# Kernel tuning notes

Measured on AMD Instinct MI355X. Metric: run time of the kernel, lower is better.

Reference implementation:

```python
import jax, jax.numpy as jnp
import numpy as np

N_ATOMS = 64
N_FEA = 64
N_RBF = 64
RBF_GAP = 0.1
N_INT = 3
BATCH = 512
P = N_ATOMS * (N_ATOMS - 1)  # 4032 ordered pairs (fully connected graph)

# pair index lists exactly as in the torch module
IDX_I = np.hstack([[k] * (N_ATOMS - 1) for k in range(N_ATOMS)])
IDX_J = np.hstack([list(range(0, k)) + list(range(k + 1, N_ATOMS)) for k in range(N_ATOMS)])


def setup_inputs() -> dict:
    key = jax.random.key(0)
    ks = jax.random.split(key, 20)
    sc_v = np.sqrt(1.0 / np.sqrt(N_FEA)).astype(np.float32)  # init scale from the module

    def lin(k, fan_in, shape):
        return jax.random.normal(k, shape, dtype=jnp.float32) / np.sqrt(fan_in)

    return {
        "r": jax.random.normal(ks[0], (BATCH, N_ATOMS * 3), dtype=jnp.float32),
        "v1": sc_v * jax.random.normal(ks[1], (N_FEA,), dtype=jnp.float32),
        "v2": sc_v * jax.random.normal(ks[2], (N_FEA,), dtype=jnp.float32),
        "rbf_centers": jnp.arange(N_RBF, dtype=jnp.float32) * 0.15625,
        # interaction-block linears, stacked over the 3 interactions; stored (in, out)
        "Wx": lin(ks[3], N_FEA, (N_INT, N_FEA, N_FEA)),
        "bx": jnp.zeros((N_INT, N_FEA), jnp.float32),
        "Wf1": lin(ks[4], N_RBF, (N_INT, N_RBF, N_FEA)),
        "bf1": jnp.zeros((N_INT, N_FEA), jnp.float32),
        "Wf2": lin(ks[5], N_FEA, (N_INT, N_FEA, N_FEA)),
        "bf2": jnp.zeros((N_INT, N_FEA), jnp.float32),
        "Wv1": lin(ks[6], N_FEA, (N_INT, N_FEA, N_FEA)),
        "bv1": jnp.zeros((N_INT, N_FEA), jnp.float32),
        "Wv2": lin(ks[7], N_FEA, (N_INT, N_FEA, N_FEA)),
        "bv2": jnp.zeros((N_INT, N_FEA), jnp.float32),
        "W1": lin(ks[8], N_FEA, (N_FEA, N_FEA // 2)),
        "b1": jnp.zeros((N_FEA // 2,), jnp.float32),
        "W2": lin(ks[9], N_FEA // 2, (N_FEA // 2, 1)),
        "b2": jnp.zeros((1,), jnp.float32),
    }


def reference(r, v1, v2, rbf_centers, Wx, bx, Wf1, bf1, Wf2, bf2,
              Wv1, bv1, Wv2, bv2, W1, b1, W2, b2):
    act = jnp.tanh
    b = r.shape[0]
    pos = r.reshape(b, N_ATOMS, 3)

    # pairwise distances (get_wrapvec = identity, no PBC)
    diff = pos[:, IDX_I] - pos[:, IDX_J]                      # (b, P, 3)
    dij = jnp.linalg.norm(diff, axis=-1, keepdims=True)       # (b, P, 1)
    rbf = jnp.exp(-(dij - rbf_centers) ** 2 / RBF_GAP)        # (b, P, R)

    # initial atom embeddings: atoms 0,1 -> v1; atoms 2.. -> v2
    x0 = jnp.concatenate([jnp.broadcast_to(v1, (2, N_FEA)),
                          jnp.broadcast_to(v2, (N_ATOMS - 2, N_FEA))], axis=0)
    X = jnp.broadcast_to(x0, (b, N_ATOMS, N_FEA))

    for t in range(N_INT):
        Xl = X @ Wx[t] + bx[t]                                # atom-wise linear
        h = act(rbf @ Wf1[t] + bf1[t])                        # filter network on RBF
        h = act(h @ Wf2[t] + bf2[t])                          # (b, P, F)
        v = h * Xl[:, IDX_J]                                  # gather neighbor feats, cfconv
        v = v.reshape(b, N_ATOMS, N_ATOMS - 1, N_FEA).sum(axis=2)  # scatter-sum over j
        v = act(v @ Wv1[t] + bv1[t])
        v = v @ Wv2[t] + bv2[t]
        X = X + v

    X = act(X @ W1 + b1)
    X = X @ W2 + b2                                           # (b, n_atoms, 1)
    return jnp.sum(X[..., 0], axis=-1, keepdims=True)         # (b, 1)
```

## Files before the change

kernel.cpp:

```cpp
#include <hip/hip_runtime.h>


typedef __attribute__((ext_vector_type(8))) __bf16 bf16x8;
typedef __attribute__((ext_vector_type(4))) __bf16 bf16x4;
typedef __attribute__((ext_vector_type(4))) float  f32x4;

#define WS_X  262144
#define WS_V  8650752
#define WS_XL 12845056

__device__ __forceinline__ int swz(int row, int byteoff) {
    return row * 128 + (byteoff ^ ((row & 7) << 4));
}

__device__ __forceinline__ float fexp2(float x) { return __builtin_amdgcn_exp2f(x); }

__device__ __forceinline__ float tanh_fast(float x) {
    float t = fexp2(2.88539008f * x);
    return fmaf(-2.0f, __builtin_amdgcn_rcpf(t + 1.0f), 1.0f);
}

struct AFrag { bf16x8 a0h, a1h, a0l, a1l; };

__device__ __forceinline__ AFrag load_afrag(const char* wsW, int mat, int wv, int lane) {
    const char* p = wsW + mat * 16384 + wv * 2048 + lane * 32;
    AFrag f;
    f.a0h = *(const bf16x8*)(p);
    f.a1h = *(const bf16x8*)(p + 16);
    f.a0l = *(const bf16x8*)(p + 8192);
    f.a1l = *(const bf16x8*)(p + 8192 + 16);
    return f;
}

template <int EPI, bool BSPLIT>
__device__ __forceinline__ void gemm64(const AFrag& A, const char* Bhi, const char* Blo,
                                       const f32x4 bv, char* Out,
                                       int lane, int wv, f32x4* ret) {
    const int l15 = lane & 15, q = lane >> 4;
    f32x4 acc[4];
#pragma unroll
    for (int nt = 0; nt < 4; ++nt) {
        const int n = 16 * nt + l15;
        const bf16x8 b0h = *(const bf16x8*)(Bhi + swz(n, 16 * q));
        const bf16x8 b1h = *(const bf16x8*)(Bhi + swz(n, 64 + 16 * q));
        f32x4 c = {0.f, 0.f, 0.f, 0.f};
        c = __builtin_amdgcn_mfma_f32_16x16x32_bf16(A.a0h, b0h, c, 0, 0, 0);
        c = __builtin_amdgcn_mfma_f32_16x16x32_bf16(A.a1h, b1h, c, 0, 0, 0);
        c = __builtin_amdgcn_mfma_f32_16x16x32_bf16(A.a0l, b0h, c, 0, 0, 0);
        c = __builtin_amdgcn_mfma_f32_16x16x32_bf16(A.a1l, b1h, c, 0, 0, 0);
        if (BSPLIT) {
            const bf16x8 b0l = *(const bf16x8*)(Blo + swz(n, 16 * q));
            const bf16x8 b1l = *(const bf16x8*)(Blo + swz(n, 64 + 16 * q));
            c = __builtin_amdgcn_mfma_f32_16x16x32_bf16(A.a0h, b0l, c, 0, 0, 0);
            c = __builtin_amdgcn_mfma_f32_16x16x32_bf16(A.a1h, b1l, c, 0, 0, 0);
        }
        acc[nt] = c;
    }
    if (EPI == 2) {
#pragma unroll
        for (int nt = 0; nt < 4; ++nt) ret[nt] = acc[nt];
        return;
    }
#pragma unroll
    for (int nt = 0; nt < 4; ++nt) {
        const int n = 16 * nt + l15;
        bf16x4 oh;
#pragma unroll
        for (int r = 0; r < 4; ++r) {
            float v = acc[nt][r] + bv[r];
            if (EPI == 1) v = tanh_fast(v);
            oh[r] = (__bf16)v;
        }
        *(bf16x4*)(Out + swz(n, 32 * wv + 8 * q)) = oh;
    }
}

__global__ void prep_weights(const float* __restrict__ Wx, const float* __restrict__ Wf1,
                             const float* __restrict__ Wf2, const float* __restrict__ Wv1,
                             const float* __restrict__ Wv2, const float* __restrict__ W1,
                             char* __restrict__ ws) {
    const int m = blockIdx.x;
    const int tid = threadIdx.x;
    const int wv = tid >> 6, lane = tid & 63;
    const int l15 = lane & 15, q = lane >> 4;
    const int m_row = 16 * wv + l15;
    const float* src;
    int wcols;
    if (m < 15) {
        const int t = m / 5, s = m % 5;
        src = (s == 0 ? Wx : s == 1 ? Wf1 : s == 2 ? Wf2 : s == 3 ? Wv1 : Wv2) + t * 4096;
        wcols = 64;
    } else {
        src = W1;
        wcols = 32;
    }
    char* base = ws + m * 16384 + wv * 2048 + lane * 32;
#pragma unroll
    for (int kc = 0; kc < 2; ++kc) {
        bf16x8 hi, lo;
#pragma unroll
        for (int e = 0; e < 8; ++e) {
            const int k = 32 * kc + 8 * q + e;
            float val = (m_row < wcols) ? src[k * wcols + m_row] : 0.0f;
            __bf16 h = (__bf16)val;
            hi[e] = h;
            lo[e] = (__bf16)(val - (float)h);
        }
        *(bf16x8*)(base + kc * 16) = hi;
        *(bf16x8*)(base + 8192 + kc * 16) = lo;
    }
}

__global__ __launch_bounds__(256, 2) void schnet_init(
    const float* __restrict__ v1g, const float* __restrict__ v2g,
    const float* __restrict__ bx,  const char* __restrict__ wsW,
    float* __restrict__ gX, __bf16* __restrict__ gXl) {
    extern __shared__ char smem[];
    char* bX   = smem;
    char* bXlo = smem + 8192;

    const int tid = threadIdx.x;
    const int lane = tid & 63, wv = tid >> 6;
    const int l15 = lane & 15, q = lane >> 4;
    const int b = blockIdx.x;

    {
        const f32x4 a1v = *(const f32x4*)(v1g + 16 * wv + 4 * q);
        const f32x4 a2v = *(const f32x4*)(v2g + 16 * wv + 4 * q);
#pragma unroll
        for (int nt = 0; nt < 4; ++nt) {
            const bool isv1 = (nt == 0) && (l15 < 2);
            bf16x4 oh, ol;
            f32x4 m;
#pragma unroll
            for (int rr = 0; rr < 4; ++rr) {
                m[rr] = isv1 ? a1v[rr] : a2v[rr];
                __bf16 h = (__bf16)m[rr];
                oh[rr] = h;
                ol[rr] = (__bf16)(m[rr] - (float)h);
            }
            const int off = swz(16 * nt + l15, 32 * wv + 8 * q);
            *(bf16x4*)(bX + off) = oh;
            *(bf16x4*)(bXlo + off) = ol;
            *(f32x4*)(gX + b * 4096 + (16 * nt + l15) * 64 + 16 * wv + 4 * q) = m;
        }
    }
    __syncthreads();
    {
        const AFrag fWx = load_afrag(wsW, 0, wv, lane);
        const f32x4 bxv = *(const f32x4*)(bx + 16 * wv + 4 * q);
        f32x4 acc[4];
        gemm64<2, true>(fWx, bX, bXlo, bxv, nullptr, lane, wv, acc);
#pragma unroll
        for (int nt = 0; nt < 4; ++nt) {
            bf16x4 oh;
#pragma unroll
            for (int rr = 0; rr < 4; ++rr) oh[rr] = (__bf16)(acc[nt][rr] + bxv[rr]);
            *(bf16x4*)(gXl + (b * 64 + 16 * nt + l15) * 64 + 16 * wv + 4 * q) = oh;
        }
    }
}

__global__ __launch_bounds__(256, 4) void schnet_a(
    const float* __restrict__ r,   const float* __restrict__ cent,
    const float* __restrict__ bf1, const float* __restrict__ bf2,
    const char* __restrict__ wsW,  const __bf16* __restrict__ gXl,
    __bf16* __restrict__ gV, int t) {
    extern __shared__ char smem[];
    char* bA  = smem;
    char* bB  = smem + 8192;
    float* sPos  = (float*)(smem + 16384);
    float* sCent = (float*)(smem + 17152);

    const int tid = threadIdx.x;
    const int lane = tid & 63, wv = tid >> 6;
    const int l15 = lane & 15, q = lane >> 4;
    const int b = blockIdx.x >> 2, qh = blockIdx.x & 3;

    if (tid < 192) sPos[(tid % 3) * 64 + tid / 3] = r[b * 192 + tid];
    if (tid < 64) sCent[tid] = cent[tid];

    const AFrag fWf1 = load_afrag(wsW, t * 5 + 1, wv, lane);
    const AFrag fWf2 = load_afrag(wsW, t * 5 + 2, wv, lane);
    const f32x4 bf1v = *(const f32x4*)(bf1 + t * 64 + 16 * wv + 4 * q);
    const f32x4 bf2v = *(const f32x4*)(bf2 + t * 64 + 16 * wv + 4 * q);

    float xlf[4][4];
#pragma unroll
    for (int nt = 0; nt < 4; ++nt) {
        const bf16x4 xl = *(const bf16x4*)(gXl + (b * 64 + 16 * nt + l15) * 64 +
                                           16 * wv + 4 * q);
#pragma unroll
        for (int r2 = 0; r2 < 4; ++r2) xlf[nt][r2] = (float)xl[r2];
    }
    __syncthreads();

    const float pjx = sPos[lane], pjy = sPos[64 + lane], pjz = sPos[128 + lane];
    const float* ccp = sCent + wv * 16;

    const int i0 = qh * 16;
    {
        const float dx = pjx - sPos[i0];
        const float dy = pjy - sPos[64 + i0];
        const float dz = pjz - sPos[128 + i0];
        const float d = __builtin_amdgcn_sqrtf(dx * dx + dy * dy + dz * dz);
        bf16x8 h0, h1v;
#pragma unroll
        for (int e = 0; e < 8; ++e) {
            float x0 = d - ccp[e];
            float x1 = d - ccp[8 + e];
            h0[e]  = (__bf16)fexp2(-14.4269504f * x0 * x0);
            h1v[e] = (__bf16)fexp2(-14.4269504f * x1 * x1);
        }
        *(bf16x8*)(bA + swz(lane, 32 * wv)) = h0;
        *(bf16x8*)(bA + swz(lane, 32 * wv + 16)) = h1v;
    }
    __syncthreads();

    for (int ii = 0; ii < 16; ++ii) {
        const int i = i0 + ii;
        gemm64<1, false>(fWf1, bA, nullptr, bf1v, bB, lane, wv, nullptr);
        __syncthreads();
        {
            f32x4 ret[4];
            gemm64<2, false>(fWf2, bB, nullptr, bf2v, nullptr, lane, wv, ret);
            float ts0 = 0.f, ts1 = 0.f, ts2 = 0.f, ts3 = 0.f;
#pragma unroll
            for (int nt = 0; nt < 4; ++nt) {
                const int j = 16 * nt + l15;
                const bool valid = (j != i);
                ts0 = fmaf(tanh_fast(ret[nt][0] + bf2v[0]), valid ? xlf[nt][0] : 0.f, ts0);
                ts1 = fmaf(tanh_fast(ret[nt][1] + bf2v[1]), valid ? xlf[nt][1] : 0.f, ts1);
                ts2 = fmaf(tanh_fast(ret[nt][2] + bf2v[2]), valid ? xlf[nt][2] : 0.f, ts2);
                ts3 = fmaf(tanh_fast(ret[nt][3] + bf2v[3]), valid ? xlf[nt][3] : 0.f, ts3);
            }
#pragma unroll
            for (int m = 1; m < 16; m <<= 1) {
                ts0 += __shfl_xor(ts0, m);
                ts1 += __shfl_xor(ts1, m);
                ts2 += __shfl_xor(ts2, m);
                ts3 += __shfl_xor(ts3, m);
            }
            if (l15 == 0) {
                bf16x4 o;
                o[0] = (__bf16)ts0; o[1] = (__bf16)ts1;
                o[2] = (__bf16)ts2; o[3] = (__bf16)ts3;
                *(bf16x4*)(gV + (b * 64 + i) * 64 + 16 * wv + 4 * q) = o;
            }
        }
        if (ii < 15) {
            const int inext = i + 1;
            const float dx = pjx - sPos[inext];
            const float dy = pjy - sPos[64 + inext];
            const float dz = pjz - sPos[128 + inext];
            const float d = __builtin_amdgcn_sqrtf(dx * dx + dy * dy + dz * dz);
            bf16x8 h0, h1v;
#pragma unroll
            for (int e = 0; e < 8; ++e) {
                float x0 = d - ccp[e];
                float x1 = d - ccp[8 + e];
                h0[e]  = (__bf16)fexp2(-14.4269504f * x0 * x0);
                h1v[e] = (__bf16)fexp2(-14.4269504f * x1 * x1);
            }
            *(bf16x8*)(bA + swz(lane, 32 * wv)) = h0;
            *(bf16x8*)(bA + swz(lane, 32 * wv + 16)) = h1v;
        }
        __syncthreads();
    }
}

__global__ __launch_bounds__(256, 2) void schnet_b(
    const float* __restrict__ bv1, const float* __restrict__ bv2,
    const float* __restrict__ bx,  const float* __restrict__ b1,
    const float* __restrict__ W2,  const float* __restrict__ b2,
    const char* __restrict__ wsW,  float* __restrict__ gX,
    const __bf16* __restrict__ gV, __bf16* __restrict__ gXl,
    float* __restrict__ out, int t) {
    extern __shared__ char smem[];
    char* bV   = smem;
    char* bB   = smem + 8192;
    char* bX   = smem + 16384;
    char* bXlo = smem + 24576;
    float* sRed = (float*)(smem + 32768);
    float* sW2v = (float*)(smem + 33280);

    const int tid = threadIdx.x;
    const int lane = tid & 63, wv = tid >> 6;
    const int l15 = lane & 15, q = lane >> 4;
    const int b = blockIdx.x;

    if (tid < 32) sW2v[tid] = W2[tid];

    {
        const int a = tid >> 2, f0 = (tid & 3) << 4;
        const __bf16* src = gV + (b * 64 + a) * 64 + f0;
        const bf16x8 v0 = *(const bf16x8*)(src);
        const bf16x8 v1 = *(const bf16x8*)(src + 8);
        *(bf16x8*)(bV + swz(a, 2 * f0)) = v0;
        *(bf16x8*)(bV + swz(a, 2 * f0 + 16)) = v1;
    }
    __syncthreads();
    {
        const AFrag fWv1 = load_afrag(wsW, t * 5 + 3, wv, lane);
        const f32x4 bv1v = *(const f32x4*)(bv1 + t * 64 + 16 * wv + 4 * q);
        gemm64<1, false>(fWv1, bV, nullptr, bv1v, bB, lane, wv, nullptr);
    }
    __syncthreads();
    f32x4 master[4];
    {
        const AFrag fWv2 = load_afrag(wsW, t * 5 + 4, wv, lane);
        f32x4 ret[4];
        gemm64<2, false>(fWv2, bB, nullptr, f32x4{0.f, 0.f, 0.f, 0.f}, nullptr,
                         lane, wv, ret);
        const f32x4 bvec = *(const f32x4*)(bv2 + t * 64 + 16 * wv + 4 * q);
#pragma unroll
        for (int nt = 0; nt < 4; ++nt) {
            float* px = gX + b * 4096 + (16 * nt + l15) * 64 + 16 * wv + 4 * q;
            f32x4 m = *(const f32x4*)px;
#pragma unroll
            for (int rr = 0; rr < 4; ++rr) m[rr] += ret[nt][rr] + bvec[rr];
            *(f32x4*)px = m;
            master[nt] = m;
            bf16x4 oh, ol;
#pragma unroll
            for (int rr = 0; rr < 4; ++rr) {
                __bf16 h = (__bf16)m[rr];
                oh[rr] = h;
                ol[rr] = (__bf16)(m[rr] - (float)h);
            }
            const int off = swz(16 * nt + l15, 32 * wv + 8 * q);
            *(bf16x4*)(bX + off) = oh;
            *(bf16x4*)(bXlo + off) = ol;
        }
    }
    __syncthreads();

    if (t < 2) {
        const AFrag fWxn = load_afrag(wsW, (t + 1) * 5 + 0, wv, lane);
        const f32x4 bxv = *(const f32x4*)(bx + (t + 1) * 64 + 16 * wv + 4 * q);
        f32x4 acc[4];
        gemm64<2, true>(fWxn, bX, bXlo, bxv, nullptr, lane, wv, acc);
#pragma unroll
        for (int nt = 0; nt < 4; ++nt) {
            bf16x4 oh;
#pragma unroll
            for (int rr = 0; rr < 4; ++rr) oh[rr] = (__bf16)(acc[nt][rr] + bxv[rr]);
            *(bf16x4*)(gXl + (b * 64 + 16 * nt + l15) * 64 + 16 * wv + 4 * q) = oh;
        }
    } else {
        if (wv < 2) {
            const AFrag fW1 = load_afrag(wsW, 15, wv, lane);
            const f32x4 b1v = *(const f32x4*)(b1 + 16 * wv + 4 * q);
            const f32x4 w2v = *(const f32x4*)(sW2v + 16 * wv + 4 * q);
#pragma unroll
            for (int nt = 0; nt < 4; ++nt) {
                const int n = 16 * nt + l15;
                const bf16x8 b0h = *(const bf16x8*)(bX + swz(n, 16 * q));
                const bf16x8 b1h = *(const bf16x8*)(bX + swz(n, 64 + 16 * q));
                const bf16x8 b0l = *(const bf16x8*)(bXlo + swz(n, 16 * q));
                const bf16x8 b1l = *(const bf16x8*)(bXlo + swz(n, 64 + 16 * q));
                f32x4 c = {0.f, 0.f, 0.f, 0.f};
                c = __builtin_amdgcn_mfma_f32_16x16x32_bf16(fW1.a0h, b0h, c, 0, 0, 0);
                c = __builtin_amdgcn_mfma_f32_16x16x32_bf16(fW1.a1h, b1h, c, 0, 0, 0);
                c = __builtin_amdgcn_mfma_f32_16x16x32_bf16(fW1.a0h, b0l, c, 0, 0, 0);
                c = __builtin_amdgcn_mfma_f32_16x16x32_bf16(fW1.a1h, b1l, c, 0, 0, 0);
                c = __builtin_amdgcn_mfma_f32_16x16x32_bf16(fW1.a0l, b0h, c, 0, 0, 0);
                c = __builtin_amdgcn_mfma_f32_16x16x32_bf16(fW1.a1l, b1h, c, 0, 0, 0);
                float p = 0.f;
#pragma unroll
                for (int rr = 0; rr < 4; ++rr)
                    p = fmaf(tanh_fast(c[rr] + b1v[rr]), w2v[rr], p);
                p += __shfl_xor(p, 16);
                p += __shfl_xor(p, 32);
                if (q == 0) sRed[wv * 64 + nt * 16 + l15] = p;
            }
        }
        __syncthreads();
        if (tid < 64) {
            float s = sRed[tid] + sRed[64 + tid];
#pragma unroll
            for (int off = 1; off < 64; off <<= 1) s += __shfl_xor(s, off);
            if (tid == 0) out[b] = s + 64.0f * b2[0];
        }
    }
}

extern "C" void kernel_launch(void* const* d_in, const int* in_sizes, int n_in,
                              void* d_out, int out_size, void* d_ws, size_t ws_size,
                              hipStream_t stream) {
    const float* r    = (const float*)d_in[0];
    const float* v1   = (const float*)d_in[1];
    const float* v2   = (const float*)d_in[2];
    const float* cent = (const float*)d_in[3];
    const float* Wx   = (const float*)d_in[4];
    const float* bx   = (const float*)d_in[5];
    const float* Wf1  = (const float*)d_in[6];
    const float* bf1  = (const float*)d_in[7];
    const float* Wf2  = (const float*)d_in[8];
    const float* bf2  = (const float*)d_in[9];
    const float* Wv1  = (const float*)d_in[10];
    const float* bv1  = (const float*)d_in[11];
    const float* Wv2  = (const float*)d_in[12];
    const float* bv2  = (const float*)d_in[13];
    const float* W1   = (const float*)d_in[14];
    const float* b1   = (const float*)d_in[15];
    const float* W2   = (const float*)d_in[16];
    const float* b2   = (const float*)d_in[17];
    char* ws = (char*)d_ws;
    float*  gX  = (float*)(ws + WS_X);
    __bf16* gV  = (__bf16*)(ws + WS_V);
    __bf16* gXl = (__bf16*)(ws + WS_XL);

    prep_weights<<<16, 256, 0, stream>>>(Wx, Wf1, Wf2, Wv1, Wv2, W1, ws);
    schnet_init<<<512, 256, 16384, stream>>>(v1, v2, bx, ws, gX, gXl);

    (void)hipFuncSetAttribute((const void*)schnet_a,
                              hipFuncAttributeMaxDynamicSharedMemorySize, 17408);
    (void)hipFuncSetAttribute((const void*)schnet_b,
                              hipFuncAttributeMaxDynamicSharedMemorySize, 33408);
    for (int t = 0; t < 3; ++t) {
        schnet_a<<<2048, 256, 17408, stream>>>(r, cent, bf1, bf2, ws, gXl, gV, t);
        schnet_b<<<512, 256, 33408, stream>>>(bv1, bv2, bx, b1, W2, b2, ws, gX,
                                              gV, gXl, (float*)d_out, t);
    }
}
```

Before: 485.3 us.

## Exploit pair symmetry to halve filter network evaluations via cyclic offsets

Reorganizes the cfconv kernel to iterate over cyclic pair offsets instead of center atoms, so each filter evaluation h_ij (symmetric in i,j) contributes to both atom i and atom j via a lane shuffle. The grid is halved and each block accumulates per-atom partial sums in registers, written as fp32 halves that the second kernel sums. This removes half of the RBF/filter GEMM and tanh work at the cost of extra gathers, cross-lane shuffles, and doubled fp32 partial-sum traffic.

After: 856.0 us. 76.4% more time.

```diff
diff --git a/kernel.cpp b/kernel.cpp
--- a/kernel.cpp
+++ b/kernel.cpp
@@ -6,8 +6,8 @@
 typedef __attribute__((ext_vector_type(4))) float  f32x4;
 
 #define WS_X  262144
-#define WS_V  8650752
-#define WS_XL 12845056
+#define WS_XL 8650752
+#define WS_VP 12845056
 
 __device__ __forceinline__ int swz(int row, int byteoff) {
     return row * 128 + (byteoff ^ ((row & 7) << 4));
@@ -165,7 +165,7 @@
     const float* __restrict__ r,   const float* __restrict__ cent,
     const float* __restrict__ bf1, const float* __restrict__ bf2,
     const char* __restrict__ wsW,  const __bf16* __restrict__ gXl,
-    __bf16* __restrict__ gV, int t) {
+    float* __restrict__ gVp, int t) {
     extern __shared__ char smem[];
     char* bA  = smem;
     char* bB  = smem + 8192;
@@ -175,7 +175,7 @@
     const int tid = threadIdx.x;
     const int lane = tid & 63, wv = tid >> 6;
     const int l15 = lane & 15, q = lane >> 4;
-    const int b = blockIdx.x >> 2, qh = blockIdx.x & 3;
+    const int b = blockIdx.x >> 1, half = blockIdx.x & 1;
 
     if (tid < 192) sPos[(tid % 3) * 64 + tid / 3] = r[b * 192 + tid];
     if (tid < 64) sCent[tid] = cent[tid];
@@ -193,80 +193,105 @@
 #pragma unroll
         for (int r2 = 0; r2 < 4; ++r2) xlf[nt][r2] = (float)xl[r2];
     }
+    f32x4 vacc[4];
+#pragma unroll
+    for (int nt = 0; nt < 4; ++nt) vacc[nt] = f32x4{0.f, 0.f, 0.f, 0.f};
     __syncthreads();
 
     const float pjx = sPos[lane], pjy = sPos[64 + lane], pjz = sPos[128 + lane];
     const float* ccp = sCent + wv * 16;
-
-    const int i0 = qh * 16;
-    {
-        const float dx = pjx - sPos[i0];
-        const float dy = pjy - sPos[64 + i0];
-        const float dz = pjz - sPos[128 + i0];
-        const float d = __builtin_amdgcn_sqrtf(dx * dx + dy * dy + dz * dz);
-        bf16x8 h0, h1v;
-#pragma unroll
-        for (int e = 0; e < 8; ++e) {
-            float x0 = d - ccp[e];
-            float x1 = d - ccp[8 + e];
-            h0[e]  = (__bf16)fexp2(-14.4269504f * x0 * x0);
-            h1v[e] = (__bf16)fexp2(-14.4269504f * x1 * x1);
-        }
-        *(bf16x8*)(bA + swz(lane, 32 * wv)) = h0;
-        *(bf16x8*)(bA + swz(lane, 32 * wv + 16)) = h1v;
-    }
-    __syncthreads();
-
-    for (int ii = 0; ii < 16; ++ii) {
-        const int i = i0 + ii;
+    const int o0 = 1 + half * 16;
+
+#define RBF_COL(O)                                                        \
+    {                                                                     \
+        const int jj = (lane + (O)) & 63;                                 \
+        const float dx = pjx - sPos[jj];                                  \
+        const float dy = pjy - sPos[64 + jj];                             \
+        const float dz = pjz - sPos[128 + jj];                            \
+        const float d = __builtin_amdgcn_sqrtf(dx * dx + dy * dy + dz * dz); \
+        bf16x8 h0, h1v;                                                   \
+        _Pragma("unroll")                                                 \
+        for (int e = 0; e < 8; ++e) {                                     \
+            float x0 = d - ccp[e];                                        \
+            float x1 = d - ccp[8 + e];                                    \
+            h0[e]  = (__bf16)fexp2(-14.4269504f * x0 * x0);               \
+            h1v[e] = (__bf16)fexp2(-14.4269504f * x1 * x1);               \
+        }                                                                 \
+        *(bf16x8*)(bA + swz(lane, 32 * wv)) = h0;                         \
+        *(bf16x8*)(bA + swz(lane, 32 * wv + 16)) = h1v;                   \
+    }
+
+    RBF_COL(o0);
+    __syncthreads();
+
+    for (int oc = 0; oc < 16; ++oc) {
+        const int o = o0 + oc;
         gemm64<1, false>(fWf1, bA, nullptr, bf1v, bB, lane, wv, nullptr);
         __syncthreads();
         {
+            bf16x4 xjl[4];
+            if (o != 32) {
+#pragma unroll
+                for (int nt = 0; nt < 4; ++nt) {
+                    const int j = (16 * nt + l15 + o) & 63;
+                    xjl[nt] = *(const bf16x4*)(gXl + (b * 64 + j) * 64 +
+                                               16 * wv + 4 * q);
+                }
+            }
             f32x4 ret[4];
             gemm64<2, false>(fWf2, bB, nullptr, bf2v, nullptr, lane, wv, ret);
-            float ts0 = 0.f, ts1 = 0.f, ts2 = 0.f, ts3 = 0.f;
-#pragma unroll
-            for (int nt = 0; nt < 4; ++nt) {
-                const int j = 16 * nt + l15;
-                const bool valid = (j != i);
-                ts0 = fmaf(tanh_fast(ret[nt][0] + bf2v[0]), valid ? xlf[nt][0] : 0.f, ts0);
-                ts1 = fmaf(tanh_fast(ret[nt][1] + bf2v[1]), valid ? xlf[nt][1] : 0.f, ts1);
-                ts2 = fmaf(tanh_fast(ret[nt][2] + bf2v[2]), valid ? xlf[nt][2] : 0.f, ts2);
-                ts3 = fmaf(tanh_fast(ret[nt][3] + bf2v[3]), valid ? xlf[nt][3] : 0.f, ts3);
+            if (o != 32) {
+                f32x4 prod[4];
+#pragma unroll
+                for (int nt = 0; nt < 4; ++nt) {
+#pragma unroll
+                    for (int r2 = 0; r2 < 4; ++r2) {
+                        const float hv = tanh_fast(ret[nt][r2] + bf2v[r2]);
+                        vacc[nt][r2] = fmaf(hv, (float)xjl[nt][r2], vacc[nt][r2]);
+                        prod[nt][r2] = hv * xlf[nt][r2];
+                    }
+                }
+                const int srcLane = (lane & 48) | ((l15 - o) & 15);
+                f32x4 rx[4];
+#pragma unroll
+                for (int nt = 0; nt < 4; ++nt)
+#pragma unroll
+                    for (int r2 = 0; r2 < 4; ++r2)
+                        rx[nt][r2] = __shfl(prod[nt][r2], srcLane, 64);
+                const int carry = (((l15 - o) & 15) + o) >> 4;
+                if (carry == 0) {
+                    vacc[0] += rx[0]; vacc[1] += rx[1];
+                    vacc[2] += rx[2]; vacc[3] += rx[3];
+                } else if (carry == 1) {
+                    vacc[1] += rx[0]; vacc[2] += rx[1];
+                    vacc[3] += rx[2]; vacc[0] += rx[3];
+                } else {
+                    vacc[2] += rx[0]; vacc[3] += rx[1];
+                    vacc[0] += rx[2]; vacc[1] += rx[3];
+                }
+            } else {
+#pragma unroll
+                for (int nt = 0; nt < 2; ++nt) {
+#pragma unroll
+                    for (int r2 = 0; r2 < 4; ++r2) {
+                        const float hv = tanh_fast(ret[nt][r2] + bf2v[r2]);
+                        vacc[nt][r2]     = fmaf(hv, xlf[nt + 2][r2], vacc[nt][r2]);
+                        vacc[nt + 2][r2] = fmaf(hv, xlf[nt][r2], vacc[nt + 2][r2]);
+                    }
+                }
             }
-#pragma unroll
-            for (int m = 1; m < 16; m <<= 1) {
-                ts0 += __shfl_xor(ts0, m);
-                ts1 += __shfl_xor(ts1, m);
-                ts2 += __shfl_xor(ts2, m);
-                ts3 += __shfl_xor(ts3, m);
-            }
-            if (l15 == 0) {
-                bf16x4 o;
-                o[0] = (__bf16)ts0; o[1] = (__bf16)ts1;
-                o[2] = (__bf16)ts2; o[3] = (__bf16)ts3;
-                *(bf16x4*)(gV + (b * 64 + i) * 64 + 16 * wv + 4 * q) = o;
-            }
-        }
-        if (ii < 15) {
-            const int inext = i + 1;
-            const float dx = pjx - sPos[inext];
-            const float dy = pjy - sPos[64 + inext];
-            const float dz = pjz - sPos[128 + inext];
-            const float d = __builtin_amdgcn_sqrtf(dx * dx + dy * dy + dz * dz);
-            bf16x8 h0, h1v;
-#pragma unroll
-            for (int e = 0; e < 8; ++e) {
-                float x0 = d - ccp[e];
-                float x1 = d - ccp[8 + e];
-                h0[e]  = (__bf16)fexp2(-14.4269504f * x0 * x0);
-                h1v[e] = (__bf16)fexp2(-14.4269504f * x1 * x1);
-            }
-            *(bf16x8*)(bA + swz(lane, 32 * wv)) = h0;
-            *(bf16x8*)(bA + swz(lane, 32 * wv + 16)) = h1v;
-        }
+        }
+        if (oc < 15) RBF_COL(o + 1);
         __syncthreads();
     }
+
+    {
+        float* dst = gVp + (half * 512 + b) * 4096;
+#pragma unroll
+        for (int nt = 0; nt < 4; ++nt)
+            *(f32x4*)(dst + (16 * nt + l15) * 64 + 16 * wv + 4 * q) = vacc[nt];
+    }
+#undef RBF_COL
 }
 
 __global__ __launch_bounds__(256, 2) void schnet_b(
@@ -274,7 +299,7 @@
     const float* __restrict__ bx,  const float* __restrict__ b1,
     const float* __restrict__ W2,  const float* __restrict__ b2,
     const char* __restrict__ wsW,  float* __restrict__ gX,
-    const __bf16* __restrict__ gV, __bf16* __restrict__ gXl,
+    const float* __restrict__ gVp, __bf16* __restrict__ gXl,
     float* __restrict__ out, int t) {
     extern __shared__ char smem[];
     char* bV   = smem;
@@ -292,12 +317,18 @@
     if (tid < 32) sW2v[tid] = W2[tid];
 
     {
-        const int a = tid >> 2, f0 = (tid & 3) << 4;
-        const __bf16* src = gV + (b * 64 + a) * 64 + f0;
-        const bf16x8 v0 = *(const bf16x8*)(src);
-        const bf16x8 v1 = *(const bf16x8*)(src + 8);
-        *(bf16x8*)(bV + swz(a, 2 * f0)) = v0;
-        *(bf16x8*)(bV + swz(a, 2 * f0 + 16)) = v1;
+        const int a2 = tid >> 2, f0 = (tid & 3) << 4;
+        const float* s0 = gVp + b * 4096 + a2 * 64 + f0;
+        const float* s1 = gVp + (512 + b) * 4096 + a2 * 64 + f0;
+#pragma unroll
+        for (int c = 0; c < 4; ++c) {
+            const f32x4 va = *(const f32x4*)(s0 + 4 * c);
+            const f32x4 vb = *(const f32x4*)(s1 + 4 * c);
+            bf16x4 o4;
+#pragma unroll
+            for (int r2 = 0; r2 < 4; ++r2) o4[r2] = (__bf16)(va[r2] + vb[r2]);
+            *(bf16x4*)(bV + swz(a2, 2 * (f0 + 4 * c))) = o4;
+        }
     }
     __syncthreads();
     {
@@ -408,8 +439,8 @@
     const float* b2   = (const float*)d_in[17];
     char* ws = (char*)d_ws;
     float*  gX  = (float*)(ws + WS_X);
-    __bf16* gV  = (__bf16*)(ws + WS_V);
     __bf16* gXl = (__bf16*)(ws + WS_XL);
+    float*  gVp = (float*)(ws + WS_VP);
 
     prep_weights<<<16, 256, 0, stream>>>(Wx, Wf1, Wf2, Wv1, Wv2, W1, ws);
     schnet_init<<<512, 256, 16384, stream>>>(v1, v2, bx, ws, gX, gXl);
@@ -419,8 +450,8 @@
     (void)hipFuncSetAttribute((const void*)schnet_b,
                               hipFuncAttributeMaxDynamicSharedMemorySize, 33408);
     for (int t = 0; t < 3; ++t) {
-        schnet_a<<<2048, 256, 17408, stream>>>(r, cent, bf1, bf2, ws, gXl, gV, t);
+        schnet_a<<<1024, 256, 17408, stream>>>(r, cent, bf1, bf2, ws, gXl, gVp, t);
         schnet_b<<<512, 256, 33408, stream>>>(bv1, bv2, bx, b1, W2, b2, ws, gX,
-                                              gV, gXl, (float*)d_out, t);
-    }
-}
+                                              gVp, gXl, (float*)d_out, t);
+    }
+}
```
